# Kernel tuning notes

Hardware: AMD Instinct MI355X
Metric: run time of the kernel (lower is better)

## Reference

```python
import jax, jax.numpy as jnp
import numpy as np

B, D_IN = 8192, 512
M0, M1 = 128, 128          # num_modules per layer
K = 8                      # topk (== module_arch[0])
H = 128                    # module hidden (module_arch[1])
T = 4                      # num_tasks
OUT = 2                    # output_dim


def setup_inputs() -> dict:
    key = jax.random.key(0)
    ks = jax.random.split(key, 16)
    s = 0.1
    return {
        "x": jax.random.normal(ks[0], (B, D_IN), jnp.float32),
        "task_id": 1,
        # routing embeddings: [num_tasks, input_dim_of_layer, num_modules]
        "emb0": jax.random.normal(ks[1], (T, D_IN, M0), jnp.float32),
        "emb1": jax.random.normal(ks[2], (T, M0, M1), jnp.float32),
        "emb_out": jax.random.normal(ks[3], (T, M1, 1), jnp.float32),
        # per-module MLP params, stacked over modules: Linear(K->H), Linear(H->1)
        "W1_0": jax.random.normal(ks[4], (M0, K, H), jnp.float32) * s,
        "b1_0": jax.random.normal(ks[5], (M0, H), jnp.float32) * s,
        "W2_0": jax.random.normal(ks[6], (M0, H), jnp.float32) * s,
        "b2_0": jax.random.normal(ks[7], (M0,), jnp.float32) * s,
        "W1_1": jax.random.normal(ks[8], (M1, K, H), jnp.float32) * s,
        "b1_1": jax.random.normal(ks[9], (M1, H), jnp.float32) * s,
        "W2_1": jax.random.normal(ks[10], (M1, H), jnp.float32) * s,
        "b2_1": jax.random.normal(ks[11], (M1,), jnp.float32) * s,
    }


def _topk_masks(emb, k, task_id):
    # emb: [T, D, M]; hard top-k one-hot masks along D (eval path of gumbel_sigmoid,
    # use_gumbel=False, hard=True). Returns [M, k, D] for the given task.
    et = jnp.transpose(emb[task_id], (1, 0))          # [M, D]
    _, idx = jax.lax.top_k(et, k)                     # [M, k]
    return jax.nn.one_hot(idx, et.shape[-1], dtype=emb.dtype)  # [M, k, D]


def _layer(x, emb, W1, b1, W2, b2, task_id):
    masks = _topk_masks(emb, K, task_id)              # [M, K, D]
    inp = jnp.einsum('bd,mkd->bmk', x, masks)         # gather routed inputs
    h = jax.nn.relu(jnp.einsum('bmk,mkh->bmh', inp, W1) + b1)  # [B, M, H]
    return jnp.einsum('bmh,mh->bm', h, W2) + b2       # [B, M]


def reference(x, task_id, emb0, emb1, emb_out,
              W1_0, b1_0, W2_0, b2_0, W1_1, b1_1, W2_1, b2_1):
    x = _layer(x, emb0, W1_0, b1_0, W2_0, b2_0, task_id)
    x = _layer(x, emb1, W1_1, b1_1, W2_1, b2_1, task_id)
    m = _topk_masks(emb_out, OUT, task_id)            # [1, OUT, M1]
    v1 = x @ m[0, 0]                                  # [B]
    v2 = x @ m[0, 1]
    return jax.nn.sigmoid(jnp.stack([v1, v2], axis=1))  # [B, 2]
```

## Files before the change

### kernel.cpp

```cpp
#include <hip/hip_runtime.h>
#include <math.h>

#define B_SZ   8192
#define D_IN   512
#define M0_N   128
#define M1_N   128
#define K_TOP  8
#define H_DIM  128
#define ROWS   16
#define XP     520


template<int NCH>
__device__ __forceinline__ void wave_topk(const float* __restrict__ base,
                                          int stride, int k, int* out_idx,
                                          int lane) {
  float v[NCH];
#pragma unroll
  for (int t = 0; t < NCH; ++t) v[t] = base[(t * 64 + lane) * stride];
  for (int r = 0; r < k; ++r) {
    float bv = -INFINITY;
    int bd = 0x7fffffff;
#pragma unroll
    for (int t = 0; t < NCH; ++t) {
      if (v[t] > bv) { bv = v[t]; bd = t * 64 + lane; }
    }
#pragma unroll
    for (int m = 1; m < 64; m <<= 1) {
      float ov = __shfl_xor(bv, m, 64);
      int   od = __shfl_xor(bd, m, 64);
      if (ov > bv || (ov == bv && od < bd)) { bv = ov; bd = od; }
    }
    if (lane == 0) out_idx[r] = bd;
    if ((bd & 63) == lane) {
      const int tw = bd >> 6;
#pragma unroll
      for (int tt = 0; tt < NCH; ++tt)
        if (tt == tw) v[tt] = -INFINITY;
    }
  }
}

__global__ __launch_bounds__(256)
void route_pre(const int* __restrict__ task_id_p,
               const float* __restrict__ emb0,
               const float* __restrict__ emb1,
               const float* __restrict__ emb_out,
               int* __restrict__ ws) {
  const int task = task_id_p[0];
  const int lane = threadIdx.x & 63;
  const int wid  = threadIdx.x >> 6;
  const int col  = blockIdx.x * 4 + wid;
  if (blockIdx.y == 0) {
    wave_topk<2>(emb1 + (size_t)task * M0_N * M1_N + col, M1_N, K_TOP,
                 ws + 64 + col * 8, lane);
    if (blockIdx.x == 0 && wid == 0)
      wave_topk<2>(emb_out + task * M1_N, 1, 2, ws, lane);
  } else {
    wave_topk<8>(emb0 + (size_t)task * D_IN * M0_N + col, M0_N, K_TOP,
                 ws + 2048 + col * 8, lane);
  }
}

__device__ __forceinline__ float dpp_add16(float p) {
  int t;
  t = __builtin_amdgcn_update_dpp(0, __float_as_int(p), 0xB1, 0xF, 0xF, true);
  p += __int_as_float(t);
  t = __builtin_amdgcn_update_dpp(0, __float_as_int(p), 0x4E, 0xF, 0xF, true);
  p += __int_as_float(t);
  t = __builtin_amdgcn_update_dpp(0, __float_as_int(p), 0x124, 0xF, 0xF, true);
  p += __int_as_float(t);
  t = __builtin_amdgcn_update_dpp(0, __float_as_int(p), 0x128, 0xF, 0xF, true);
  p += __int_as_float(t);
  return p;
}

__device__ __forceinline__ float slice8(const float4* w1a, const float4* w1b,
                                        const float4& b1a, const float4& b1b,
                                        const float4& w2a, const float4& w2b,
                                        const float* xv) {
  float4 h0 = b1a, h1 = b1b;
#pragma unroll
  for (int k = 0; k < 8; ++k) {
    h0.x = fmaf(xv[k], w1a[k].x, h0.x);
    h0.y = fmaf(xv[k], w1a[k].y, h0.y);
    h0.z = fmaf(xv[k], w1a[k].z, h0.z);
    h0.w = fmaf(xv[k], w1a[k].w, h0.w);
    h1.x = fmaf(xv[k], w1b[k].x, h1.x);
    h1.y = fmaf(xv[k], w1b[k].y, h1.y);
    h1.z = fmaf(xv[k], w1b[k].z, h1.z);
    h1.w = fmaf(xv[k], w1b[k].w, h1.w);
  }
  float pa = 0.f, pb = 0.f;
  pa = fmaf(fmaxf(h0.x, 0.f), w2a.x, pa);
  pa = fmaf(fmaxf(h0.y, 0.f), w2a.y, pa);
  pa = fmaf(fmaxf(h0.z, 0.f), w2a.z, pa);
  pa = fmaf(fmaxf(h0.w, 0.f), w2a.w, pa);
  pb = fmaf(fmaxf(h1.x, 0.f), w2b.x, pb);
  pb = fmaf(fmaxf(h1.y, 0.f), w2b.y, pb);
  pb = fmaf(fmaxf(h1.z, 0.f), w2b.z, pb);
  pb = fmaf(fmaxf(h1.w, 0.f), w2b.w, pb);
  return dpp_add16(pa + pb);
}

__global__ __launch_bounds__(256, 2)
void fused_compute(const float* __restrict__ x,
                   const float* __restrict__ W1_0, const float* __restrict__ b1_0,
                   const float* __restrict__ W2_0, const float* __restrict__ b2_0,
                   const float* __restrict__ W1_1, const float* __restrict__ b1_1,
                   const float* __restrict__ W2_1, const float* __restrict__ b2_1,
                   const int* __restrict__ ws, float* __restrict__ out) {
  __shared__ __align__(16) float xt[ROWS * XP];
  __shared__ int   s_m1[2];
  __shared__ int   s_m0[16];
  __shared__ int   s_cols[128];
  __shared__ float tile[16 * 18];

  const int tid  = threadIdx.x;
  const int wid  = tid >> 6;
  const int lane = tid & 63;
  const int rowbase = blockIdx.x * ROWS;

#pragma unroll
  for (int i = 0; i < 8; ++i) {
    const int chunk = wid * 8 + i;
    const int row   = chunk >> 1;
    const int half  = chunk & 1;
    const float* gsrc = x + (size_t)(rowbase + row) * D_IN + half * 256 +
                        lane * 4;
    float* ldst = xt + row * XP + half * 256;
    __builtin_amdgcn_global_load_lds(
        (const __attribute__((address_space(1))) void*)gsrc,
        (__attribute__((address_space(3))) void*)ldst, 16, 0, 0);
  }

  if (tid < 128) {
    const int slot = tid >> 3, k = tid & 7;
    const int m1 = ws[slot >> 3];
    const int m0 = ws[64 + m1 * 8 + (slot & 7)];
    if (k == 0) s_m0[slot] = m0;
    s_cols[tid] = ws[2048 + m0 * 8 + k];
    if (tid < 2) s_m1[tid] = ws[tid];
  }
  __syncthreads();

  const int g  = lane & 15;
  const int rq = lane >> 4;

#pragma unroll
  for (int si = 0; si < 4; ++si) {
    const int s  = wid * 4 + si;
    const int m0 = s_m0[s];
    const float4* w1p = (const float4*)(W1_0 + (size_t)m0 * (K_TOP * H_DIM));
    float4 w1a[8], w1b[8];
#pragma unroll
    for (int k = 0; k < 8; ++k) {
      w1a[k] = w1p[k * 32 + 2 * g];
      w1b[k] = w1p[k * 32 + 2 * g + 1];
    }
    const float4 b1a = ((const float4*)(b1_0 + m0 * H_DIM))[2 * g];
    const float4 b1b = ((const float4*)(b1_0 + m0 * H_DIM))[2 * g + 1];
    const float4 w2a = ((const float4*)(W2_0 + m0 * H_DIM))[2 * g];
    const float4 w2b = ((const float4*)(W2_0 + m0 * H_DIM))[2 * g + 1];
    const float  b2v = b2_0[m0];
    int cols[8];
#pragma unroll
    for (int k = 0; k < 8; ++k) cols[k] = s_cols[s * 8 + k];

#pragma unroll
    for (int it = 0; it < 4; ++it) {
      const int r = it * 4 + rq;
      const float* xrow = xt + r * XP;
      float xv[8];
#pragma unroll
      for (int k = 0; k < 8; ++k) xv[k] = xrow[cols[k]];
      const float p = slice8(w1a, w1b, b1a, b1b, w2a, w2b, xv);
      if (g == 0) tile[s * 18 + r] = p + b2v;
    }
  }
  __syncthreads();

  {
    const int j  = wid & 1;
    const int rh = wid >> 1;
    const int m1 = s_m1[j];
    const float4* w1p = (const float4*)(W1_1 + (size_t)m1 * (K_TOP * H_DIM));
    float4 w1a[8], w1b[8];
#pragma unroll
    for (int k = 0; k < 8; ++k) {
      w1a[k] = w1p[k * 32 + 2 * g];
      w1b[k] = w1p[k * 32 + 2 * g + 1];
    }
    const float4 b1a = ((const float4*)(b1_1 + m1 * H_DIM))[2 * g];
    const float4 b1b = ((const float4*)(b1_1 + m1 * H_DIM))[2 * g + 1];
    const float4 w2a = ((const float4*)(W2_1 + m1 * H_DIM))[2 * g];
    const float4 w2b = ((const float4*)(W2_1 + m1 * H_DIM))[2 * g + 1];
    const float  b2v = b2_1[m1];

#pragma unroll
    for (int it = 0; it < 2; ++it) {
      const int r = rh * 8 + it * 4 + rq;
      float xv[8];
#pragma unroll
      for (int k = 0; k < 8; ++k) xv[k] = tile[(j * 8 + k) * 18 + r];
      const float p = slice8(w1a, w1b, b1a, b1b, w2a, w2b, xv);
      if (g == 0) {
        const float v = p + b2v;
        out[(size_t)(rowbase + r) * 2 + j] = 1.f / (1.f + __expf(-v));
      }
    }
  }
}

extern "C" void kernel_launch(void* const* d_in, const int* in_sizes, int n_in,
                              void* d_out, int out_size, void* d_ws, size_t ws_size,
                              hipStream_t stream) {
  const float* x       = (const float*)d_in[0];
  const int*   task_id = (const int*)  d_in[1];
  const float* emb0    = (const float*)d_in[2];
  const float* emb1    = (const float*)d_in[3];
  const float* emb_out = (const float*)d_in[4];
  const float* W1_0    = (const float*)d_in[5];
  const float* b1_0    = (const float*)d_in[6];
  const float* W2_0    = (const float*)d_in[7];
  const float* b2_0    = (const float*)d_in[8];
  const float* W1_1    = (const float*)d_in[9];
  const float* b1_1    = (const float*)d_in[10];
  const float* W2_1    = (const float*)d_in[11];
  const float* b2_1    = (const float*)d_in[12];

  int* ws = (int*)d_ws;

  route_pre<<<dim3(32, 2), 256, 0, stream>>>(task_id, emb0, emb1, emb_out, ws);
  fused_compute<<<B_SZ / ROWS, 256, 0, stream>>>(x, W1_0, b1_0, W2_0, b2_0,
                                                 W1_1, b1_1, W2_1, b2_1,
                                                 ws, (float*)d_out);
}
```

Baseline: 23.95 us.

## Make each wave own its rows end-to-end and drop block barriers

Restructures the fused kernel so each wave loads its own 4 rows of x into LDS and computes all 16 layer-0 modules for those rows, keeping the results in registers. It then feeds them straight into the two layer-1 modules, removing the shared routing tables, the intermediate LDS tile and both __syncthreads. The trade is that every wave now loads all 16 modules' W1 weights (four times more per-block weight traffic, mostly served from cache) and holds a larger register working set.

```diff
diff --git a/kernel.cpp b/kernel.cpp
--- a/kernel.cpp
+++ b/kernel.cpp
@@ -111,21 +111,17 @@
                    const float* __restrict__ W2_1, const float* __restrict__ b2_1,
                    const int* __restrict__ ws, float* __restrict__ out) {
   __shared__ __align__(16) float xt[ROWS * XP];
-  __shared__ int   s_m1[2];
-  __shared__ int   s_m0[16];
-  __shared__ int   s_cols[128];
-  __shared__ float tile[16 * 18];
 
   const int tid  = threadIdx.x;
   const int wid  = tid >> 6;
   const int lane = tid & 63;
   const int rowbase = blockIdx.x * ROWS;
+  const int r0 = wid * 4;
 
 #pragma unroll
   for (int i = 0; i < 8; ++i) {
-    const int chunk = wid * 8 + i;
-    const int row   = chunk >> 1;
-    const int half  = chunk & 1;
+    const int row  = r0 + (i >> 1);
+    const int half = i & 1;
     const float* gsrc = x + (size_t)(rowbase + row) * D_IN + half * 256 +
                         lane * 4;
     float* ldst = xt + row * XP + half * 256;
@@ -134,23 +130,30 @@
         (__attribute__((address_space(3))) void*)ldst, 16, 0, 0);
   }
 
-  if (tid < 128) {
-    const int slot = tid >> 3, k = tid & 7;
-    const int m1 = ws[slot >> 3];
-    const int m0 = ws[64 + m1 * 8 + (slot & 7)];
-    if (k == 0) s_m0[slot] = m0;
-    s_cols[tid] = ws[2048 + m0 * 8 + k];
-    if (tid < 2) s_m1[tid] = ws[tid];
-  }
-  __syncthreads();
+  int m1j[2];
+  m1j[0] = ws[0];
+  m1j[1] = ws[1];
+  int m0s[16];
+#pragma unroll
+  for (int s = 0; s < 16; ++s)
+    m0s[s] = ws[64 + m1j[s >> 3] * 8 + (s & 7)];
+
+  asm volatile("s_waitcnt vmcnt(0)" ::: "memory");
+  __builtin_amdgcn_sched_barrier(0);
 
   const int g  = lane & 15;
   const int rq = lane >> 4;
-
-#pragma unroll
-  for (int si = 0; si < 4; ++si) {
-    const int s  = wid * 4 + si;
-    const int m0 = s_m0[s];
+  const float* xrow = xt + (r0 + rq) * XP;
+
+  float res[16];
+#pragma unroll
+  for (int s = 0; s < 16; ++s) {
+    const int m0 = m0s[s];
+    const int* cp = ws + 2048 + m0 * 8;
+    int cols[8];
+#pragma unroll
+    for (int k = 0; k < 8; ++k) cols[k] = cp[k];
+
     const float4* w1p = (const float4*)(W1_0 + (size_t)m0 * (K_TOP * H_DIM));
     float4 w1a[8], w1b[8];
 #pragma unroll
@@ -163,27 +166,17 @@
     const float4 w2a = ((const float4*)(W2_0 + m0 * H_DIM))[2 * g];
     const float4 w2b = ((const float4*)(W2_0 + m0 * H_DIM))[2 * g + 1];
     const float  b2v = b2_0[m0];
-    int cols[8];
-#pragma unroll
-    for (int k = 0; k < 8; ++k) cols[k] = s_cols[s * 8 + k];
-
-#pragma unroll
-    for (int it = 0; it < 4; ++it) {
-      const int r = it * 4 + rq;
-      const float* xrow = xt + r * XP;
-      float xv[8];
-#pragma unroll
-      for (int k = 0; k < 8; ++k) xv[k] = xrow[cols[k]];
-      const float p = slice8(w1a, w1b, b1a, b1b, w2a, w2b, xv);
-      if (g == 0) tile[s * 18 + r] = p + b2v;
-    }
-  }
-  __syncthreads();
-
-  {
-    const int j  = wid & 1;
-    const int rh = wid >> 1;
-    const int m1 = s_m1[j];
+
+    float xv[8];
+#pragma unroll
+    for (int k = 0; k < 8; ++k) xv[k] = xrow[cols[k]];
+
+    res[s] = slice8(w1a, w1b, b1a, b1b, w2a, w2b, xv) + b2v;
+  }
+
+#pragma unroll
+  for (int j = 0; j < 2; ++j) {
+    const int m1 = m1j[j];
     const float4* w1p = (const float4*)(W1_1 + (size_t)m1 * (K_TOP * H_DIM));
     float4 w1a[8], w1b[8];
 #pragma unroll
@@ -197,17 +190,14 @@
     const float4 w2b = ((const float4*)(W2_1 + m1 * H_DIM))[2 * g + 1];
     const float  b2v = b2_1[m1];
 
-#pragma unroll
-    for (int it = 0; it < 2; ++it) {
-      const int r = rh * 8 + it * 4 + rq;
-      float xv[8];
-#pragma unroll
-      for (int k = 0; k < 8; ++k) xv[k] = tile[(j * 8 + k) * 18 + r];
-      const float p = slice8(w1a, w1b, b1a, b1b, w2a, w2b, xv);
-      if (g == 0) {
-        const float v = p + b2v;
-        out[(size_t)(rowbase + r) * 2 + j] = 1.f / (1.f + __expf(-v));
-      }
+    float xv[8];
+#pragma unroll
+    for (int k = 0; k < 8; ++k) xv[k] = res[j * 8 + k];
+
+    const float p = slice8(w1a, w1b, b1a, b1b, w2a, w2b, xv);
+    if (g == 0) {
+      const float v = p + b2v;
+      out[(size_t)(rowbase + r0 + rq) * 2 + j] = 1.f / (1.f + __expf(-v));
     }
   }
 }
```

Measured after the change: 37.13 us. +55.0%, slower.

## Resolve routing per wave and double-buffer layer-0 module weights in registers

Applied to the files above, without the earlier changes.

Each wave now reads its routing indices (m1, m0, gathered columns) straight from the workspace into wave-uniform registers, dropping the shared-memory staging and one barrier. It then preloads weights for two modules before the barrier that waits on the x tile load, and prefetches the next module's weights while computing the current one. The goal is to hide global-load latency of the per-module weights behind the x load and the FMA work. This doubles the weight register footprint, which under launch_bounds(256,2) risks spills or lower occupancy.

```diff
diff --git a/kernel.cpp b/kernel.cpp
--- a/kernel.cpp
+++ b/kernel.cpp
@@ -103,6 +103,30 @@
   return dpp_add16(pa + pb);
 }
 
+struct WSet {
+  float4 w1a[8], w1b[8];
+  float4 b1a, b1b, w2a, w2b;
+  float  b2;
+};
+
+__device__ __forceinline__ void loadW(WSet& S, int m0,
+                                      const float* __restrict__ W1,
+                                      const float* __restrict__ b1,
+                                      const float* __restrict__ W2,
+                                      const float* __restrict__ b2, int g) {
+  const float4* w1p = (const float4*)(W1 + (size_t)m0 * (K_TOP * H_DIM));
+#pragma unroll
+  for (int k = 0; k < 8; ++k) {
+    S.w1a[k] = w1p[k * 32 + 2 * g];
+    S.w1b[k] = w1p[k * 32 + 2 * g + 1];
+  }
+  S.b1a = ((const float4*)(b1 + m0 * H_DIM))[2 * g];
+  S.b1b = ((const float4*)(b1 + m0 * H_DIM))[2 * g + 1];
+  S.w2a = ((const float4*)(W2 + m0 * H_DIM))[2 * g];
+  S.w2b = ((const float4*)(W2 + m0 * H_DIM))[2 * g + 1];
+  S.b2  = b2[m0];
+}
+
 __global__ __launch_bounds__(256, 2)
 void fused_compute(const float* __restrict__ x,
                    const float* __restrict__ W1_0, const float* __restrict__ b1_0,
@@ -111,19 +135,16 @@
                    const float* __restrict__ W2_1, const float* __restrict__ b2_1,
                    const int* __restrict__ ws, float* __restrict__ out) {
   __shared__ __align__(16) float xt[ROWS * XP];
-  __shared__ int   s_m1[2];
-  __shared__ int   s_m0[16];
-  __shared__ int   s_cols[128];
   __shared__ float tile[16 * 18];
 
   const int tid  = threadIdx.x;
-  const int wid  = tid >> 6;
   const int lane = tid & 63;
+  const int uwid = __builtin_amdgcn_readfirstlane(tid >> 6);
   const int rowbase = blockIdx.x * ROWS;
 
 #pragma unroll
   for (int i = 0; i < 8; ++i) {
-    const int chunk = wid * 8 + i;
+    const int chunk = uwid * 8 + i;
     const int row   = chunk >> 1;
     const int half  = chunk & 1;
     const float* gsrc = x + (size_t)(rowbase + row) * D_IN + half * 256 +
@@ -134,38 +155,35 @@
         (__attribute__((address_space(3))) void*)ldst, 16, 0, 0);
   }
 
-  if (tid < 128) {
-    const int slot = tid >> 3, k = tid & 7;
-    const int m1 = ws[slot >> 3];
-    const int m0 = ws[64 + m1 * 8 + (slot & 7)];
-    if (k == 0) s_m0[slot] = m0;
-    s_cols[tid] = ws[2048 + m0 * 8 + k];
-    if (tid < 2) s_m1[tid] = ws[tid];
-  }
-  __syncthreads();
+  const int m1A = ws[0];
+  const int m1B = ws[1];
+  int m0s[4];
+  int cols[4][8];
+#pragma unroll
+  for (int si = 0; si < 4; ++si) {
+    const int s  = uwid * 4 + si;
+    const int m1 = (s < 8) ? m1A : m1B;
+    m0s[si] = ws[64 + m1 * 8 + (s & 7)];
+#pragma unroll
+    for (int k = 0; k < 8; ++k) cols[si][k] = ws[2048 + m0s[si] * 8 + k];
+  }
 
   const int g  = lane & 15;
   const int rq = lane >> 4;
 
+  WSet A, B;
+  loadW(A, m0s[0], W1_0, b1_0, W2_0, b2_0, g);
+  loadW(B, m0s[1], W1_0, b1_0, W2_0, b2_0, g);
+
+  __syncthreads();
+
 #pragma unroll
   for (int si = 0; si < 4; ++si) {
-    const int s  = wid * 4 + si;
-    const int m0 = s_m0[s];
-    const float4* w1p = (const float4*)(W1_0 + (size_t)m0 * (K_TOP * H_DIM));
-    float4 w1a[8], w1b[8];
-#pragma unroll
-    for (int k = 0; k < 8; ++k) {
-      w1a[k] = w1p[k * 32 + 2 * g];
-      w1b[k] = w1p[k * 32 + 2 * g + 1];
-    }
-    const float4 b1a = ((const float4*)(b1_0 + m0 * H_DIM))[2 * g];
-    const float4 b1b = ((const float4*)(b1_0 + m0 * H_DIM))[2 * g + 1];
-    const float4 w2a = ((const float4*)(W2_0 + m0 * H_DIM))[2 * g];
-    const float4 w2b = ((const float4*)(W2_0 + m0 * H_DIM))[2 * g + 1];
-    const float  b2v = b2_0[m0];
-    int cols[8];
-#pragma unroll
-    for (int k = 0; k < 8; ++k) cols[k] = s_cols[s * 8 + k];
+    const WSet& S = (si & 1) ? B : A;
+    const int sg = uwid * 4 + si;
+    int cv[8];
+#pragma unroll
+    for (int k = 0; k < 8; ++k) cv[k] = cols[si][k];
 
 #pragma unroll
     for (int it = 0; it < 4; ++it) {
@@ -173,29 +191,21 @@
       const float* xrow = xt + r * XP;
       float xv[8];
 #pragma unroll
-      for (int k = 0; k < 8; ++k) xv[k] = xrow[cols[k]];
-      const float p = slice8(w1a, w1b, b1a, b1b, w2a, w2b, xv);
-      if (g == 0) tile[s * 18 + r] = p + b2v;
-    }
+      for (int k = 0; k < 8; ++k) xv[k] = xrow[cv[k]];
+      const float p = slice8(S.w1a, S.w1b, S.b1a, S.b1b, S.w2a, S.w2b, xv);
+      if (g == 0) tile[sg * 18 + r] = p + S.b2;
+    }
+    if (si == 0) loadW(A, m0s[2], W1_0, b1_0, W2_0, b2_0, g);
+    if (si == 1) loadW(B, m0s[3], W1_0, b1_0, W2_0, b2_0, g);
   }
   __syncthreads();
 
   {
-    const int j  = wid & 1;
-    const int rh = wid >> 1;
-    const int m1 = s_m1[j];
-    const float4* w1p = (const float4*)(W1_1 + (size_t)m1 * (K_TOP * H_DIM));
-    float4 w1a[8], w1b[8];
-#pragma unroll
-    for (int k = 0; k < 8; ++k) {
-      w1a[k] = w1p[k * 32 + 2 * g];
-      w1b[k] = w1p[k * 32 + 2 * g + 1];
-    }
-    const float4 b1a = ((const float4*)(b1_1 + m1 * H_DIM))[2 * g];
-    const float4 b1b = ((const float4*)(b1_1 + m1 * H_DIM))[2 * g + 1];
-    const float4 w2a = ((const float4*)(W2_1 + m1 * H_DIM))[2 * g];
-    const float4 w2b = ((const float4*)(W2_1 + m1 * H_DIM))[2 * g + 1];
-    const float  b2v = b2_1[m1];
+    const int j  = uwid & 1;
+    const int rh = uwid >> 1;
+    const int m1 = j ? m1B : m1A;
+    WSet L;
+    loadW(L, m1, W1_1, b1_1, W2_1, b2_1, g);
 
 #pragma unroll
     for (int it = 0; it < 2; ++it) {
@@ -203,9 +213,9 @@
       float xv[8];
 #pragma unroll
       for (int k = 0; k < 8; ++k) xv[k] = tile[(j * 8 + k) * 18 + r];
-      const float p = slice8(w1a, w1b, b1a, b1b, w2a, w2b, xv);
+      const float p = slice8(L.w1a, L.w1b, L.b1a, L.b1b, L.w2a, L.w2b, xv);
       if (g == 0) {
-        const float v = p + b2v;
+        const float v = p + L.b2;
         out[(size_t)(rowbase + r) * 2 + j] = 1.f / (1.f + __expf(-v));
       }
     }
```

Measured after the change: 23.78 us. About the same (-0.7%).
